# Performance work log

Hardware: AMD Instinct MI355X
Metric: run time of the kernel (lower is better)

Reference implementation:

```python
import jax, jax.numpy as jnp
import numpy as np

N_QUBITS = 14
DEPTH = 8
NUM_BLOCKS = DEPTH // 2
BATCH = 256
INIT_SCALE = 0.1


def _ry_mat(theta):
    # RY(t) = [[cos(t/2), -sin(t/2)], [sin(t/2), cos(t/2)]]; works for scalar or batched theta
    c = jnp.cos(theta / 2).astype(jnp.complex64)
    s = jnp.sin(theta / 2).astype(jnp.complex64)
    return jnp.stack([jnp.stack([c, -s], -1), jnp.stack([s, c], -1)], -2)


def _rz_mat(theta):
    # RZ(t) = diag(exp(-i t/2), exp(+i t/2))
    e = jnp.exp(-0.5j * theta.astype(jnp.complex64))
    z = jnp.zeros_like(e)
    return jnp.stack([jnp.stack([e, z], -1), jnp.stack([z, jnp.conj(e)], -1)], -2)


def _rx_mat(theta):
    # RX(t) = [[cos(t/2), -i sin(t/2)], [-i sin(t/2), cos(t/2)]] (target block of CRX)
    c = jnp.cos(theta / 2).astype(jnp.complex64)
    s = (-1j) * jnp.sin(theta / 2).astype(jnp.complex64)
    return jnp.stack([jnp.stack([c, s], -1), jnp.stack([s, c], -1)], -2)


def _apply_1q(state, mat, q, n):
    # state: (B, 2**n) complex64. Wire 0 = most significant axis (PennyLane convention).
    B = state.shape[0]
    s = state.reshape(B, 2 ** q, 2, 2 ** (n - q - 1))
    if mat.ndim == 3:  # per-sample angles (input encoding layer)
        out = jnp.einsum('bij,bljr->blir', mat, s)
    else:
        out = jnp.einsum('ij,bljr->blir', mat, s)
    return out.reshape(B, -1)


def _apply_ctrl(state, mat, c, t, n):
    # Apply 2x2 `mat` on target wire t where control wire c == 1.
    B = state.shape[0]
    s = state.reshape(B, 2 ** c, 2, 2 ** (n - c - 1))
    sub = s[:, :, 1, :]  # control = |1> subspace, (B, 2**c, 2**(n-c-1))
    p = t if t < c else t - 1  # target position in the reduced (n-1)-qubit register
    sub2 = sub.reshape(B, 2 ** p, 2, 2 ** (n - 2 - p))
    sub2 = jnp.einsum('ij,bljr->blir', mat, sub2)
    return s.at[:, :, 1, :].set(sub2.reshape(sub.shape)).reshape(B, -1)


def _circuit(inputs, weights):
    n, nb = N_QUBITS, NUM_BLOCKS
    B = inputs.shape[0]
    state = jnp.zeros((B, 2 ** n), jnp.complex64).at[:, 0].set(1.0)
    # input encoding: RY(inputs[..., q]) on each wire (batched angles)
    for q in range(n):
        state = _apply_1q(state, _ry_mat(inputs[:, q]), q, n)
    # weights flat index = b*3n + layer*n + q  ->  reshape (nb, 3, n)
    w = weights.reshape(nb, 3, n)
    X = jnp.asarray([[0, 1], [1, 0]], dtype=jnp.complex64)

    def block(st, wb):
        for q in range(n):
            st = _apply_1q(st, _ry_mat(wb[0, q]), q, n)
        for q in range(n):
            st = _apply_ctrl(st, X, q, (q + 1) % n, n)  # CNOT ring
        for q in range(n):
            st = _apply_1q(st, _rz_mat(wb[1, q]), q, n)
        for q in range(n):
            st = _apply_ctrl(st, _rx_mat(wb[2, q]), q, (q + 1) % n, n)  # CRX ring
        return st

    block = jax.checkpoint(block)
    for b in range(nb):
        state = block(state, w[b])

    # <Z_q> = P(bit_q = 0) - P(bit_q = 1)
    probs = state.real ** 2 + state.imag ** 2
    outs = []
    for q in range(n):
        pq = probs.reshape(B, 2 ** q, 2, -1)
        outs.append(pq[:, :, 0, :].sum((1, 2)) - pq[:, :, 1, :].sum((1, 2)))
    return jnp.stack(outs, -1).astype(jnp.float32)


def setup_inputs() -> dict:
    key = jax.random.key(0)
    k1, k2 = jax.random.split(key)
    inputs = jax.random.normal(k1, (BATCH, N_QUBITS), dtype=jnp.float32)
    weights = INIT_SCALE * jax.random.normal(k2, (3 * N_QUBITS * NUM_BLOCKS,), dtype=jnp.float32)
    return {"inputs": inputs, "weights": weights}


def reference(inputs, weights):
    return _circuit(inputs, weights)
```

## Files before the change

kernel.cpp:

```cpp
#include <hip/hip_runtime.h>
#include <utility>

#define NQ 14
#define NST (1 << NQ)
#define THREADS 512
#define NP 16
#define NE 32

typedef float f2 __attribute__((ext_vector_type(2)));

struct PassD {
    unsigned short comboR[NE];
    unsigned short rows[5];
    unsigned short tmask[5];
    unsigned short crx_widx[4];
    unsigned short ry_widx[4];
    unsigned char  ry_tb[4];
    unsigned char  ncrx;
    unsigned char  nry;
    short          rzidx;
    unsigned char  measfold;
};
struct RZD  { unsigned short rows_ng[9]; unsigned short widx_ng[9]; unsigned short widx_g[5]; };
struct AllD { PassD pass[NP]; RZD rz[4]; unsigned short meas_rows_ng[9]; int npass; };

constexpr void fill_geom(PassD& P, const unsigned short* R, const unsigned short* C, const int* tb)
{
    for (int i = 0; i < 5; ++i) { P.tmask[i] = C[tb[i]]; P.rows[i] = R[tb[i]]; }
    for (int j = 0; j < NE; ++j) {
        unsigned short x = 0;
        for (int i = 0; i < 5; ++i) if ((j >> i) & 1) x = (unsigned short)(x ^ P.tmask[i]);
        P.comboR[j] = x;
    }
}

constexpr void ring(unsigned short* R, unsigned short* C) {
    for (int q = 0; q < NQ; ++q) {
        int cb = 13 - q, tb = 13 - ((q + 1) % NQ);
        R[tb] = (unsigned short)(R[tb] ^ R[cb]);
        C[cb] = (unsigned short)(C[cb] ^ C[tb]);
    }
}

constexpr AllD build_desc() {
    AllD A{};
    unsigned short R[NQ] = {}, C[NQ] = {};
    for (int k = 0; k < NQ; ++k) { R[k] = (unsigned short)(1u << k); C[k] = (unsigned short)(1u << k); }
    int np = 0;
    const int tiles[4][5]  = {{13,12,11,10,9},{9,8,7,6,5},{5,4,3,2,1},{1,0,13,3,2}};
    const int gfirst[4]    = {0, 4, 8, 12};
    const int ngate[4]     = {4, 4, 4, 2};
    const int rybits[4][4] = {{12,11,10,0},{9,8,7,6},{5,4,3,2},{13,1,0,0}};
    const int nryp[4]      = {3, 4, 4, 3};

    for (int blk = 0; blk < 4; ++blk) {
        ring(R, C);
        for (int pi = 0; pi < 4; ++pi) {
            PassD& P = A.pass[np];
            fill_geom(P, R, C, tiles[pi]);
            P.ncrx = (unsigned char)ngate[pi];
            for (int g = 0; g < 4; ++g)
                P.crx_widx[g] = (unsigned short)((g < ngate[pi]) ? blk*42 + 28 + gfirst[pi] + g : 0);
            if (blk < 3) {
                P.nry = (unsigned char)nryp[pi];
                for (int g = 0; g < 4; ++g) {
                    if (g < nryp[pi]) {
                        int k = rybits[pi][g];
                        P.ry_widx[g] = (unsigned short)((blk + 1)*42 + (13 - k));
                        int t = 0;
                        for (int i = 0; i < 5; ++i) if (tiles[pi][i] == k) t = i;
                        P.ry_tb[g] = (unsigned char)t;
                    } else { P.ry_widx[g] = 0; P.ry_tb[g] = 0; }
                }
            } else { P.nry = 0; for (int g = 0; g < 4; ++g) { P.ry_widx[g] = 0; P.ry_tb[g] = 0; } }
            P.rzidx = (short)((pi == 0) ? blk : -1);
            P.measfold = (unsigned char)((blk == 3 && pi == 3) ? 1 : 0);
            if (pi == 0) {
                RZD& Z = A.rz[blk];
                for (int i = 0; i < 5; ++i)
                    Z.widx_g[i] = (unsigned short)(blk*42 + 14 + (13 - tiles[0][i]));
                int t = 0;
                for (int q = 5; q < NQ; ++q, ++t) {
                    Z.rows_ng[t] = R[13 - q];
                    Z.widx_ng[t] = (unsigned short)(blk*42 + 14 + q);
                }
            }
            ++np;
        }
        if (blk == 3)
            for (int t = 0; t < 9; ++t) A.meas_rows_ng[t] = R[13 - (1 + t)];
    }
    A.npass = np;
    return A;
}

constexpr AllD A = build_desc();
static_assert(A.npass == NP, "expected 16 passes");

constexpr int parity14(unsigned v) { v ^= v >> 8; v ^= v >> 4; v ^= v >> 2; v ^= v >> 1; return (int)(v & 1); }

constexpr bool check_dual() {
    for (int p = 0; p < NP; ++p)
        for (int i = 0; i < 5; ++i)
            for (int j = 0; j < 5; ++j)
                if (parity14((unsigned)(A.pass[p].rows[i] & A.pass[p].tmask[j])) != (i == j ? 1 : 0))
                    return false;
    return true;
}
static_assert(check_dual(), "R/C duality violated");

struct GWT { unsigned short w[NP][8]; };
constexpr GWT build_gwt() {
    GWT g{};
    for (int p = 0; p < NP; ++p) {
        for (int s = 0; s < 4; ++s) g.w[p][s]     = A.pass[p].crx_widx[s];
        for (int s = 0; s < 4; ++s) g.w[p][4 + s] = A.pass[p].ry_widx[s];
    }
    return g;
}
constexpr GWT GW = build_gwt();

constexpr int lead(unsigned short v) { int b = 13; while (b > 0 && !((v >> b) & 1)) --b; return b; }

struct Span {
    unsigned short red[14]; int n;
    constexpr unsigned short reduce(unsigned short v) const {
        for (int i = 0; i < n; ++i) { int lb = lead(red[i]); if ((v >> lb) & 1) v = (unsigned short)(v ^ red[i]); }
        return v;
    }
    constexpr bool add(unsigned short v) {
        unsigned short r = reduce(v);
        if (!r) return false;
        red[n++] = r; return true;
    }
};

constexpr unsigned short proj(unsigned short vec, const PassD& P) {
    unsigned short r = vec;
    for (int t = 0; t < 5; ++t)
        if (parity14((unsigned)(vec & P.rows[t]))) r = (unsigned short)(r ^ P.tmask[t]);
    return r;
}

struct VecsT { unsigned short lane[NP][6]; unsigned short g[NP/2][3]; int ok; };
constexpr VecsT build_vecs() {
    VecsT V{}; V.ok = 1;
    for (int k = 0; k < NP/2; ++k) {
        const PassD& P0 = A.pass[2*k];
        const PassD& P1 = A.pass[2*k + 1];
        Span SW{}; unsigned short Wb[11] = {}; int nw = 0;
        for (int i = 0; i < 5; ++i) if (SW.add(P0.tmask[i])) Wb[nw++] = P0.tmask[i];
        for (int i = 0; i < 5; ++i) if (nw < 11 && SW.add(P1.tmask[i])) Wb[nw++] = P1.tmask[i];
        for (int b = 0; b < 14 && nw < 11; ++b) {
            unsigned short e = (unsigned short)(1u << b);
            if (SW.add(e)) Wb[nw++] = e;
        }
        if (nw != 11) V.ok = 0;
        Span SG = SW; int ngv = 0;
        for (int b = 0; b < 14 && ngv < 3; ++b) {
            unsigned short e = (unsigned short)(1u << b);
            if (SG.add(e)) V.g[k][ngv++] = e;
        }
        if (ngv != 3) V.ok = 0;
        for (int pp = 0; pp < 2; ++pp) {
            const PassD& P = (pp == 0) ? P0 : P1;
            int pidx = 2*k + pp;
            Span ST{};
            for (int i = 0; i < 5; ++i) ST.add(P.tmask[i]);
            int nl = 0;
            for (int i = 0; i < 11 && nl < 6; ++i)
                if (ST.add(Wb[i])) V.lane[pidx][nl++] = Wb[i];
            if (nl != 6) V.ok = 0;
            Span SF{};
            for (int i = 0; i < 5; ++i) SF.add(P.tmask[i]);
            for (int i = 0; i < 6; ++i) if (!SF.add(V.lane[pidx][i])) V.ok = 0;
            for (int i = 0; i < 3; ++i) if (!SF.add(V.g[k][i])) V.ok = 0;
            if (SF.n != 14) V.ok = 0;
        }
    }
    return V;
}
constexpr VecsT VC = build_vecs();
static_assert(VC.ok == 1, "vec construction failed");

struct P6T { unsigned short u[NP][6]; };
constexpr P6T build_p6() {
    P6T X{};
    for (int p = 0; p < NP; ++p)
        for (int i = 0; i < 6; ++i)
            X.u[p][i] = proj(VC.lane[p][i], A.pass[p]);
    return X;
}
constexpr P6T P6 = build_p6();

constexpr unsigned lmap(const unsigned short* row, unsigned x) {
    unsigned l = 0;
    for (int t = 0; t < 4; ++t) l |= (unsigned)parity14(row[t] & x) << t;
    return l;
}
constexpr int nib_rank(const unsigned* nibs, int n) {
    unsigned basis[4] = {};
    int r = 0;
    for (int i = 0; i < n; ++i) {
        unsigned v = nibs[i] & 15u;
        for (int b = 3; b >= 0 && v; --b) {
            if (!((v >> b) & 1)) continue;
            if (basis[b]) v ^= basis[b];
            else { basis[b] = v; ++r; v = 0; }
        }
    }
    return r;
}
struct Lp { unsigned short row[4]; int score; };

constexpr int full_score(const unsigned short* r) {
    unsigned cn[4] = {};
    for (int c = 0; c < 4; ++c) {
        unsigned v = 0;
        for (int t = 0; t < 4; ++t) v |= ((unsigned)(r[t] >> c) & 1u) << t;
        cn[c] = v;
    }
    if (nib_rank(cn, 4) != 4) return -1;
    int sc = 0;
    for (int p = 0; p < NP; ++p) {
        unsigned im[6] = {};
        for (int i = 0; i < 6; ++i) im[i] = lmap(r, P6.u[p][i]);
        if (nib_rank(im, 6) == 4) ++sc;
    }
    return sc;
}

constexpr Lp search_stage(unsigned seed, int iters) {
    Lp best{}; best.score = -1;
    unsigned s = seed;
    for (int it = 0; it < iters; ++it) {
        unsigned short r[4] = {};
        for (int t = 0; t < 4; ++t) { s = s*1664525u + 1013904223u; r[t] = (unsigned short)((s >> 9) & 0x3FFF); }
        int sc = full_score(r);
        if (sc > best.score) { best.score = sc; for (int t = 0; t < 4; ++t) best.row[t] = r[t]; }
        if (best.score == NP) break;
    }
    return best;
}
constexpr Lp S0 = search_stage(0x12345u, 400);
constexpr Lp S1 = search_stage(0xBEEF1u, 400);
constexpr Lp S2 = search_stage(0xC0FFEu, 400);
constexpr Lp S3 = search_stage(0x777A1u, 400);
constexpr Lp S4 = search_stage(0x51DE5u, 400);
constexpr Lp S5 = search_stage(0xA11CEu, 400);
constexpr Lp S6 = search_stage(0x0F00Du, 400);
constexpr Lp S7 = search_stage(0x13579u, 400);
constexpr Lp pick_best() {
    Lp b = S0;
    if (S1.score > b.score) b = S1;
    if (S2.score > b.score) b = S2;
    if (S3.score > b.score) b = S3;
    if (S4.score > b.score) b = S4;
    if (S5.score > b.score) b = S5;
    if (S6.score > b.score) b = S6;
    if (S7.score > b.score) b = S7;
    return b;
}
constexpr Lp climb(Lp start, int sweeps) {
    Lp cur = start;
    for (int sw = 0; sw < sweeps && cur.score < NP; ++sw) {
        for (int t = 0; t < 4; ++t) {
            for (int b = 0; b < 14; ++b) {
                if (cur.score >= NP) break;
                unsigned short nr[4] = {cur.row[0], cur.row[1], cur.row[2], cur.row[3]};
                nr[t] = (unsigned short)(nr[t] ^ (1u << b));
                int sc = full_score(nr);
                if (sc > cur.score) { cur.score = sc; cur.row[t] = nr[t]; }
            }
        }
    }
    return cur;
}
constexpr Lp C0 = climb(pick_best(), 2);
constexpr Lp C1 = climb(C0, 2);
constexpr Lp LSEL = C1;
static_assert(LSEL.score >= 13, "bank-map search failed badly");

constexpr unsigned short swz2(unsigned short x) {
    return (unsigned short)(((unsigned)x & ~15u) | lmap(LSEL.row, x));
}

constexpr int add_basis4(unsigned* basis, unsigned v) {
    for (int b = 3; b >= 0; --b) {
        if (!((v >> b) & 1)) continue;
        if (basis[b]) v ^= basis[b];
        else { basis[b] = v; return 1; }
    }
    return 0;
}
constexpr int add_basis6(unsigned* basis, unsigned v) {
    for (int b = 5; b >= 0; --b) {
        if (!((v >> b) & 1)) continue;
        if (basis[b]) v ^= basis[b];
        else { basis[b] = v; return 1; }
    }
    return 0;
}
struct LaneOrd { unsigned short lane[NP][6]; };
constexpr LaneOrd build_lane2() {
    LaneOrd O{};
    for (int p = 0; p < NP; ++p) {
        for (int i = 0; i < 6; ++i) O.lane[p][i] = VC.lane[p][i];
        unsigned imu[6] = {};
        for (int i = 0; i < 6; ++i) imu[i] = lmap(LSEL.row, P6.u[p][i]);
        {
            unsigned chk[6] = {imu[0], imu[1], imu[2], imu[3], imu[4], imu[5]};
            if (nib_rank(chk, 6) != 4) continue;
        }
        unsigned short nl[6] = {};
        int ns = 0;
        unsigned ib[4] = {};
        unsigned sb[6] = {};
        for (unsigned c = 1; c < 64 && ns < 4; ++c) {
            unsigned img = 0; unsigned short rv = 0;
            for (int i = 0; i < 6; ++i) if ((c >> i) & 1) { img ^= imu[i]; rv = (unsigned short)(rv ^ VC.lane[p][i]); }
            if (img == 0) continue;
            unsigned ib2[4] = {ib[0], ib[1], ib[2], ib[3]};
            unsigned sb2[6] = {sb[0], sb[1], sb[2], sb[3], sb[4], sb[5]};
            if (add_basis4(ib2, img) && add_basis6(sb2, c)) {
                for (int t = 0; t < 4; ++t) ib[t] = ib2[t];
                for (int t = 0; t < 6; ++t) sb[t] = sb2[t];
                nl[ns++] = rv;
            }
        }
        for (unsigned c = 1; c < 64 && ns < 6; ++c) {
            unsigned img = 0; unsigned short rv = 0;
            for (int i = 0; i < 6; ++i) if ((c >> i) & 1) { img ^= imu[i]; rv = (unsigned short)(rv ^ VC.lane[p][i]); }
            if (img != 0) continue;
            unsigned sb2[6] = {sb[0], sb[1], sb[2], sb[3], sb[4], sb[5]};
            if (add_basis6(sb2, c)) {
                for (int t = 0; t < 6; ++t) sb[t] = sb2[t];
                nl[ns++] = rv;
            }
        }
        if (ns == 6)
            for (int i = 0; i < 6; ++i) O.lane[p][i] = nl[i];
    }
    return O;
}
constexpr LaneOrd LO = build_lane2();

struct CS2 { unsigned short c[NP][NE]; };
constexpr CS2 build_cs2() {
    CS2 C{};
    for (int p = 0; p < NP; ++p)
        for (int j = 0; j < NE; ++j)
            C.c[p][j] = swz2(A.pass[p].comboR[j]);
    return C;
}
constexpr CS2 CSS = build_cs2();

struct LJt { unsigned short v[NE]; };
constexpr LJt build_lj() {
    LJt t{};
    for (int j = 0; j < NE; ++j) t.v[j] = (unsigned short)lmap(LSEL.row, (unsigned)(j * THREADS));
    return t;
}
constexpr LJt LJ = build_lj();

constexpr unsigned pack_entry(unsigned short vec0, int p) {
    const PassD& P = A.pass[p];
    unsigned short vec = proj(vec0, P);
    unsigned par = 0;
    if (P.rzidx >= 0)
        for (int t = 0; t < 9; ++t) par |= (unsigned)parity14(vec & A.rz[P.rzidx].rows_ng[t]) << t;
    if (P.measfold)
        for (int t = 0; t < 9; ++t) par |= (unsigned)parity14(vec & A.meas_rows_ng[t]) << t;
    return ((unsigned)swz2(vec) << 3) | (par << 22);
}

struct LutsT { unsigned v[NP][2][32]; };
constexpr LutsT build_luts() {
    LutsT L{};
    for (int p = 0; p < NP; ++p) {
        int k = p >> 1;
        for (int t = 0; t < 32; ++t) {
            unsigned short x = 0;
            for (int i = 0; i < 5; ++i) if ((t >> i) & 1) x = (unsigned short)(x ^ LO.lane[p][i]);
            L.v[p][0][t] = pack_entry(x, p);
        }
        for (int t = 0; t < 16; ++t) {
            unsigned short y = 0;
            if (t & 1) y = (unsigned short)(y ^ LO.lane[p][5]);
            for (int i = 0; i < 3; ++i) if ((t >> (i + 1)) & 1) y = (unsigned short)(y ^ VC.g[k][i]);
            L.v[p][1][t] = pack_entry(y, p);
        }
    }
    return L;
}
constexpr LutsT LUTS = build_luts();
__device__ __constant__ LutsT cLUTS = LUTS;

template<int Pi>
__device__ __forceinline__ void run_pass(f2* st, const f2 (*tabG)[8], const float (*tabRZ)[14],
                                         unsigned comb, float* acc)
{
    constexpr PassD Pd = A.pass[Pi];
    char* stb = (char*)st;
    const int base = (int)(comb & 0x1FFF8u);
    const unsigned par = comb >> 22;

    f2 v[NE];
#pragma unroll
    for (int j = 0; j < NE; ++j)
        v[j] = *(const f2*)(stb + (base ^ (CSS.c[Pi][j] << 3)));

    if constexpr (Pd.rzidx >= 0) {
        float phi0 = 0.f;
#pragma unroll
        for (int t = 0; t < 9; ++t) {
            float h = tabRZ[Pd.rzidx][t];
            phi0 += ((par >> t) & 1) ? h : -h;
        }
        const float h0 = tabRZ[Pd.rzidx][9],  h1 = tabRZ[Pd.rzidx][10];
        const float h2 = tabRZ[Pd.rzidx][11], h3 = tabRZ[Pd.rzidx][12];
        const float h4 = tabRZ[Pd.rzidx][13];
#pragma unroll
        for (int j = 0; j < NE; ++j) {
            float phi = (((((phi0 + ((j & 1) ? h0 : -h0)) + ((j & 2) ? h1 : -h1))
                                  + ((j & 4) ? h2 : -h2)) + ((j & 8) ? h3 : -h3))
                                  + ((j & 16) ? h4 : -h4));
            float s, c; __sincosf(phi, &s, &c);
            f2 C = {c, c}, S = {-s, s};
            v[j] = C * v[j] + S * v[j].yx;
        }
    }

#pragma unroll
    for (int g = 0; g < Pd.ncrx; ++g) {
        f2 cs = tabG[Pi][g];
        f2 C = {cs.x, cs.x}, S = {cs.y, -cs.y};
#pragma unroll
        for (int j = 0; j < NE; ++j) if (((j >> g) & 1) && !((j >> (g + 1)) & 1)) {
            int j1 = j | (1 << (g + 1));
            f2 a0 = v[j], a1 = v[j1];
            v[j]  = C * a0 + S * a1.yx;
            v[j1] = C * a1 + S * a0.yx;
        }
    }

#pragma unroll
    for (int g = 0; g < Pd.nry; ++g) {
        int t = Pd.ry_tb[g];
        f2 cs = tabG[Pi][4 + g];
        f2 C = {cs.x, cs.x}, Sv = {cs.y, cs.y}, NS = {-cs.y, -cs.y};
#pragma unroll
        for (int j = 0; j < NE; ++j) if (!((j >> t) & 1)) {
            int j1 = j | (1 << t);
            f2 a0 = v[j], a1 = v[j1];
            v[j]  = C * a0 + NS * a1;
            v[j1] = Sv * a0 + C * a1;
        }
    }

    if constexpr (Pd.measfold != 0) {
        f2 ps = {0.f, 0.f}, p0 = {0.f, 0.f}, p1 = {0.f, 0.f}, p2 = {0.f, 0.f}, p3 = {0.f, 0.f}, p4 = {0.f, 0.f};
#pragma unroll
        for (int j = 0; j < NE; ++j) {
            f2 t2 = v[j] * v[j];
            ps += t2;
            if (j & 1)  p0 += t2;
            if (j & 2)  p1 += t2;
            if (j & 4)  p2 += t2;
            if (j & 8)  p3 += t2;
            if (j & 16) p4 += t2;
        }
        float psum = ps.x + ps.y;
        float pg0 = p0.x + p0.y, pg1 = p1.x + p1.y, pg2 = p2.x + p2.y;
        float pg3 = p3.x + p3.y, pg4 = p4.x + p4.y;
        acc[12] += psum - 2.f * pg0;
        acc[13] += psum - 2.f * pg1;
        acc[0]  += psum - 2.f * pg2;
        acc[10] += psum - 2.f * pg3;
        acc[11] += psum - 2.f * pg4;
#pragma unroll
        for (int t = 0; t < 9; ++t) {
            float sg = ((par >> t) & 1) ? -1.f : 1.f;
            acc[1 + t] += sg * psum;
        }
    } else {
#pragma unroll
        for (int j = 0; j < NE; ++j)
            *(f2*)(stb + (base ^ (CSS.c[Pi][j] << 3))) = v[j];
        if constexpr ((Pi & 1) != 0) __syncthreads();
    }
}

template<int... I>
__device__ __forceinline__ void run_all(std::integer_sequence<int, I...>,
                                        f2* st, const f2 (*tabG)[8], const float (*tabRZ)[14],
                                        const unsigned* comb, float* acc)
{
    (run_pass<I>(st, tabG, tabRZ, comb[I], acc), ...);
}

__global__ __launch_bounds__(THREADS, 2)
void qsim_kernel(const float* __restrict__ inputs,
                 const float* __restrict__ weights,
                 float* __restrict__ out)
{
    __shared__ f2     st[NST];
    __shared__ float  tab[256];
    __shared__ f2     tabG[NP][8];
    __shared__ float  tabRZ[4][14];
    __shared__ float  red[THREADS / 64][NQ];

    const int b = blockIdx.x;
    const int tid = threadIdx.x;

    unsigned comb[NP];
#pragma unroll
    for (int p = 0; p < NP; ++p)
        comb[p] = cLUTS.v[p][0][tid & 31] ^ cLUTS.v[p][1][tid >> 5];

    if (tid < 128) {
        int p = tid >> 3, sl = tid & 7;
        float w = weights[GW.w[p][sl]];
        float s, c; __sincosf(0.5f * w, &s, &c);
        tabG[p][sl] = (f2){c, s};
    } else if (tid >= 128 && tid < 128 + 56) {
        int idx = tid - 128;
        int blk = idx / 14, k = idx - blk * 14;
        unsigned wi = (k < 9) ? A.rz[blk].widx_ng[k] : A.rz[blk].widx_g[k - 9];
        tabRZ[blk][k] = 0.5f * weights[wi];
    } else if (tid >= 256) {
        int t = tid - 256;
        int half = t >> 7, tt = t & 127;
        float prod = 1.f;
#pragma unroll
        for (int j = 0; j < 7; ++j) {
            int xb = j + 7 * half;
            int q  = 13 - xb;
            float a = 0.5f * (inputs[b * NQ + q] + weights[q]);
            float s, c; __sincosf(a, &s, &c);
            prod *= ((tt >> j) & 1) ? s : c;
        }
        tab[t] = prod;
    }
    __syncthreads();

    unsigned l4t = 0;
#pragma unroll
    for (int t = 0; t < 4; ++t)
        l4t |= (unsigned)(__popc((int)(LSEL.row[t] & tid)) & 1) << t;
#pragma unroll
    for (int j = 0; j < NE; ++j) {
        int x = tid + j * THREADS;
        int addr = (x & ~15) | (int)(l4t ^ LJ.v[j]);
        st[addr] = (f2){tab[x & 127] * tab[128 + (x >> 7)], 0.f};
    }
    __syncthreads();

    float acc[NQ];
#pragma unroll
    for (int q = 0; q < NQ; ++q) acc[q] = 0.f;

    run_all(std::make_integer_sequence<int, NP>{}, st, tabG, tabRZ, comb, acc);

#pragma unroll
    for (int q = 0; q < NQ; ++q) {
        float v2 = acc[q];
        v2 += __shfl_down(v2, 32);
        v2 += __shfl_down(v2, 16);
        v2 += __shfl_down(v2, 8);
        v2 += __shfl_down(v2, 4);
        v2 += __shfl_down(v2, 2);
        v2 += __shfl_down(v2, 1);
        acc[q] = v2;
    }
    const int wave = tid >> 6, lane = tid & 63;
    if (lane == 0) {
#pragma unroll
        for (int q = 0; q < NQ; ++q) red[wave][q] = acc[q];
    }
    __syncthreads();
    if (tid < NQ) {
        float v2 = 0.f;
#pragma unroll
        for (int w = 0; w < THREADS / 64; ++w) v2 += red[w][tid];
        out[b * NQ + tid] = v2;
    }
}

extern "C" void kernel_launch(void* const* d_in, const int* in_sizes, int n_in,
                              void* d_out, int out_size, void* d_ws, size_t ws_size,
                              hipStream_t stream) {
    const float* inputs  = (const float*)d_in[0];
    const float* weights = (const float*)d_in[1];
    float* out = (float*)d_out;
    const int B = in_sizes[0] / NQ;
    qsim_kernel<<<dim3(B), dim3(THREADS), 0, stream>>>(inputs, weights, out);
}
```

Before: 42.97 us.

## Double threads per block, halve per-thread amplitudes, use cross-lane shuffle for fifth tile bit

Each block now uses 1024 threads with 16 amplitudes per thread instead of 512 threads with 32. The fifth tile qubit of each pass is mapped to a lane bit, so the last CRX gate pairs amplitudes across lanes with __shfl_xor. Its RZ phase and Z measurement contribution come from a per-lane parity bit stored in the lookup table. This is meant to cut register pressure and raise occupancy and latency hiding, at the cost of shuffle traffic and larger block-wide barriers.

```diff
diff --git a/kernel.cpp b/kernel.cpp
--- a/kernel.cpp
+++ b/kernel.cpp
@@ -3,9 +3,9 @@
 
 #define NQ 14
 #define NST (1 << NQ)
-#define THREADS 512
+#define THREADS 1024
 #define NP 16
-#define NE 32
+#define NE 16
 
 typedef float f2 __attribute__((ext_vector_type(2)));
 
@@ -29,7 +29,7 @@
     for (int i = 0; i < 5; ++i) { P.tmask[i] = C[tb[i]]; P.rows[i] = R[tb[i]]; }
     for (int j = 0; j < NE; ++j) {
         unsigned short x = 0;
-        for (int i = 0; i < 5; ++i) if ((j >> i) & 1) x = (unsigned short)(x ^ P.tmask[i]);
+        for (int i = 0; i < 4; ++i) if ((j >> i) & 1) x = (unsigned short)(x ^ P.tmask[i]);
         P.comboR[j] = x;
     }
 }
@@ -109,6 +109,14 @@
 }
 static_assert(check_dual(), "R/C duality violated");
 
+constexpr bool check_ry() {
+    for (int p = 0; p < NP; ++p)
+        for (int g = 0; g < A.pass[p].nry; ++g)
+            if (A.pass[p].ry_tb[g] > 3) return false;
+    return true;
+}
+static_assert(check_ry(), "RY fold on lane bit not supported");
+
 struct GWT { unsigned short w[NP][8]; };
 constexpr GWT build_gwt() {
     GWT g{};
@@ -137,44 +145,46 @@
 
 constexpr unsigned short proj(unsigned short vec, const PassD& P) {
     unsigned short r = vec;
-    for (int t = 0; t < 5; ++t)
+    for (int t = 0; t < 4; ++t)
         if (parity14((unsigned)(vec & P.rows[t]))) r = (unsigned short)(r ^ P.tmask[t]);
     return r;
 }
 
-struct VecsT { unsigned short lane[NP][6]; unsigned short g[NP/2][3]; int ok; };
+struct VecsT { unsigned short lane[NP][6]; unsigned short g[NP/2][4]; int ok; };
 constexpr VecsT build_vecs() {
     VecsT V{}; V.ok = 1;
     for (int k = 0; k < NP/2; ++k) {
         const PassD& P0 = A.pass[2*k];
         const PassD& P1 = A.pass[2*k + 1];
-        Span SW{}; unsigned short Wb[11] = {}; int nw = 0;
+        Span SW{}; unsigned short Wb[10] = {}; int nw = 0;
         for (int i = 0; i < 5; ++i) if (SW.add(P0.tmask[i])) Wb[nw++] = P0.tmask[i];
-        for (int i = 0; i < 5; ++i) if (nw < 11 && SW.add(P1.tmask[i])) Wb[nw++] = P1.tmask[i];
-        for (int b = 0; b < 14 && nw < 11; ++b) {
+        for (int i = 0; i < 5; ++i) if (nw < 10 && SW.add(P1.tmask[i])) Wb[nw++] = P1.tmask[i];
+        for (int b = 0; b < 14 && nw < 10; ++b) {
             unsigned short e = (unsigned short)(1u << b);
             if (SW.add(e)) Wb[nw++] = e;
         }
-        if (nw != 11) V.ok = 0;
+        if (nw != 10) V.ok = 0;
         Span SG = SW; int ngv = 0;
-        for (int b = 0; b < 14 && ngv < 3; ++b) {
+        for (int b = 0; b < 14 && ngv < 4; ++b) {
             unsigned short e = (unsigned short)(1u << b);
             if (SG.add(e)) V.g[k][ngv++] = e;
         }
-        if (ngv != 3) V.ok = 0;
+        if (ngv != 4) V.ok = 0;
         for (int pp = 0; pp < 2; ++pp) {
             const PassD& P = (pp == 0) ? P0 : P1;
             int pidx = 2*k + pp;
             Span ST{};
-            for (int i = 0; i < 5; ++i) ST.add(P.tmask[i]);
+            for (int i = 0; i < 4; ++i) ST.add(P.tmask[i]);
             int nl = 0;
-            for (int i = 0; i < 11 && nl < 6; ++i)
+            if (ST.add(P.tmask[4])) V.lane[pidx][nl++] = P.tmask[4];
+            else V.ok = 0;
+            for (int i = 0; i < 10 && nl < 6; ++i)
                 if (ST.add(Wb[i])) V.lane[pidx][nl++] = Wb[i];
             if (nl != 6) V.ok = 0;
             Span SF{};
-            for (int i = 0; i < 5; ++i) SF.add(P.tmask[i]);
+            for (int i = 0; i < 4; ++i) SF.add(P.tmask[i]);
             for (int i = 0; i < 6; ++i) if (!SF.add(V.lane[pidx][i])) V.ok = 0;
-            for (int i = 0; i < 3; ++i) if (!SF.add(V.g[k][i])) V.ok = 0;
+            for (int i = 0; i < 4; ++i) if (!SF.add(V.g[k][i])) V.ok = 0;
             if (SF.n != 14) V.ok = 0;
         }
     }
@@ -345,6 +355,25 @@
 }
 constexpr LaneOrd LO = build_lane2();
 
+struct SHMt { int m[NP]; int ok; };
+constexpr SHMt build_shm() {
+    SHMt S{}; S.ok = 1;
+    for (int p = 0; p < NP; ++p) {
+        S.m[p] = 0;
+        if (A.pass[p].ncrx < 4) continue;
+        int found = 0;
+        for (unsigned c = 1; c < 64 && !found; ++c) {
+            unsigned short x = 0;
+            for (int i = 0; i < 6; ++i) if ((c >> i) & 1) x = (unsigned short)(x ^ LO.lane[p][i]);
+            if (x == A.pass[p].tmask[4]) { S.m[p] = (int)c; found = 1; }
+        }
+        if (!found) S.ok = 0;
+    }
+    return S;
+}
+constexpr SHMt SHM = build_shm();
+static_assert(SHM.ok == 1, "shuffle mask not found");
+
 struct CS2 { unsigned short c[NP][NE]; };
 constexpr CS2 build_cs2() {
     CS2 C{};
@@ -371,6 +400,7 @@
         for (int t = 0; t < 9; ++t) par |= (unsigned)parity14(vec & A.rz[P.rzidx].rows_ng[t]) << t;
     if (P.measfold)
         for (int t = 0; t < 9; ++t) par |= (unsigned)parity14(vec & A.meas_rows_ng[t]) << t;
+    par |= (unsigned)parity14(vec & P.rows[4]) << 9;
     return ((unsigned)swz2(vec) << 3) | (par << 22);
 }
 
@@ -383,11 +413,9 @@
             unsigned short x = 0;
             for (int i = 0; i < 5; ++i) if ((t >> i) & 1) x = (unsigned short)(x ^ LO.lane[p][i]);
             L.v[p][0][t] = pack_entry(x, p);
-        }
-        for (int t = 0; t < 16; ++t) {
             unsigned short y = 0;
             if (t & 1) y = (unsigned short)(y ^ LO.lane[p][5]);
-            for (int i = 0; i < 3; ++i) if ((t >> (i + 1)) & 1) y = (unsigned short)(y ^ VC.g[k][i]);
+            for (int i = 0; i < 4; ++i) if ((t >> (i + 1)) & 1) y = (unsigned short)(y ^ VC.g[k][i]);
             L.v[p][1][t] = pack_entry(y, p);
         }
     }
@@ -417,14 +445,13 @@
             float h = tabRZ[Pd.rzidx][t];
             phi0 += ((par >> t) & 1) ? h : -h;
         }
+        { float h = tabRZ[Pd.rzidx][13]; phi0 += ((par >> 9) & 1) ? h : -h; }
         const float h0 = tabRZ[Pd.rzidx][9],  h1 = tabRZ[Pd.rzidx][10];
         const float h2 = tabRZ[Pd.rzidx][11], h3 = tabRZ[Pd.rzidx][12];
-        const float h4 = tabRZ[Pd.rzidx][13];
 #pragma unroll
         for (int j = 0; j < NE; ++j) {
-            float phi = (((((phi0 + ((j & 1) ? h0 : -h0)) + ((j & 2) ? h1 : -h1))
-                                  + ((j & 4) ? h2 : -h2)) + ((j & 8) ? h3 : -h3))
-                                  + ((j & 16) ? h4 : -h4));
+            float phi = ((((phi0 + ((j & 1) ? h0 : -h0)) + ((j & 2) ? h1 : -h1))
+                                 + ((j & 4) ? h2 : -h2)) + ((j & 8) ? h3 : -h3));
             float s, c; __sincosf(phi, &s, &c);
             f2 C = {c, c}, S = {-s, s};
             v[j] = C * v[j] + S * v[j].yx;
@@ -432,7 +459,7 @@
     }
 
 #pragma unroll
-    for (int g = 0; g < Pd.ncrx; ++g) {
+    for (int g = 0; g < (Pd.ncrx < 3 ? (int)Pd.ncrx : 3); ++g) {
         f2 cs = tabG[Pi][g];
         f2 C = {cs.x, cs.x}, S = {cs.y, -cs.y};
 #pragma unroll
@@ -443,6 +470,18 @@
             v[j1] = C * a1 + S * a0.yx;
         }
     }
+    if constexpr (Pd.ncrx == 4) {
+        constexpr int sm = SHM.m[Pi];
+        f2 cs = tabG[Pi][3];
+        f2 C = {cs.x, cs.x}, S = {cs.y, -cs.y};
+#pragma unroll
+        for (int j = 8; j < 16; ++j) {
+            f2 pv;
+            pv.x = __shfl_xor(v[j].x, sm, 64);
+            pv.y = __shfl_xor(v[j].y, sm, 64);
+            v[j] = C * v[j] + S * pv.yx;
+        }
+    }
 
 #pragma unroll
     for (int g = 0; g < Pd.nry; ++g) {
@@ -459,25 +498,24 @@
     }
 
     if constexpr (Pd.measfold != 0) {
-        f2 ps = {0.f, 0.f}, p0 = {0.f, 0.f}, p1 = {0.f, 0.f}, p2 = {0.f, 0.f}, p3 = {0.f, 0.f}, p4 = {0.f, 0.f};
+        f2 ps = {0.f, 0.f}, p0 = {0.f, 0.f}, p1 = {0.f, 0.f}, p2 = {0.f, 0.f}, p3 = {0.f, 0.f};
 #pragma unroll
         for (int j = 0; j < NE; ++j) {
             f2 t2 = v[j] * v[j];
             ps += t2;
-            if (j & 1)  p0 += t2;
-            if (j & 2)  p1 += t2;
-            if (j & 4)  p2 += t2;
-            if (j & 8)  p3 += t2;
-            if (j & 16) p4 += t2;
+            if (j & 1) p0 += t2;
+            if (j & 2) p1 += t2;
+            if (j & 4) p2 += t2;
+            if (j & 8) p3 += t2;
         }
         float psum = ps.x + ps.y;
-        float pg0 = p0.x + p0.y, pg1 = p1.x + p1.y, pg2 = p2.x + p2.y;
-        float pg3 = p3.x + p3.y, pg4 = p4.x + p4.y;
+        float pg0 = p0.x + p0.y, pg1 = p1.x + p1.y, pg2 = p2.x + p2.y, pg3 = p3.x + p3.y;
         acc[12] += psum - 2.f * pg0;
         acc[13] += psum - 2.f * pg1;
         acc[0]  += psum - 2.f * pg2;
         acc[10] += psum - 2.f * pg3;
-        acc[11] += psum - 2.f * pg4;
+        float s4 = ((par >> 9) & 1) ? -1.f : 1.f;
+        acc[11] += s4 * psum;
 #pragma unroll
         for (int t = 0; t < 9; ++t) {
             float sg = ((par >> t) & 1) ? -1.f : 1.f;
@@ -499,7 +537,7 @@
     (run_pass<I>(st, tabG, tabRZ, comb[I], acc), ...);
 }
 
-__global__ __launch_bounds__(THREADS, 2)
+__global__ __launch_bounds__(THREADS, 4)
 void qsim_kernel(const float* __restrict__ inputs,
                  const float* __restrict__ weights,
                  float* __restrict__ out)
@@ -528,7 +566,7 @@
         int blk = idx / 14, k = idx - blk * 14;
         unsigned wi = (k < 9) ? A.rz[blk].widx_ng[k] : A.rz[blk].widx_g[k - 9];
         tabRZ[blk][k] = 0.5f * weights[wi];
-    } else if (tid >= 256) {
+    } else if (tid >= 256 && tid < 512) {
         int t = tid - 256;
         int half = t >> 7, tt = t & 127;
         float prod = 1.f;
```

After: 47.88 us. 11.4% more time.
